# Performance work log

Measured on AMD Instinct MI355X. Metric: run time of the kernel, lower is better.

The kernel has to match this reference:

```python
import jax, jax.numpy as jnp
import numpy as np

B, T, C, HS = 8, 4096, 1024, 128
BLOCK = 4096  # block_size; T == BLOCK here


def _pyr_mask(bs):
    # Faithful numpy translation of the torch 'pyr' buffer construction.
    h = bs // 2
    top = np.repeat(np.flip(np.tril(np.ones((h, h), np.float32)), axis=1), 2, axis=0)  # (bs, h)
    reps = np.array([2] * (h - 1) + [1])
    bot = np.concatenate(
        [np.zeros((1, h), np.float32),
         np.repeat(np.tril(np.ones((h, h), np.float32)), reps, axis=0)], axis=0)  # (bs, h)
    return np.concatenate([top, bot], axis=1)  # (bs, bs)


def setup_inputs() -> dict:
    key = jax.random.key(0)
    kx, kq, kk, kv = jax.random.split(key, 4)
    s = C ** -0.5
    x = jax.random.normal(kx, (B, T, C), jnp.float32)
    Wq = jax.random.normal(kq, (C, HS), jnp.float32) * s
    Wk = jax.random.normal(kk, (C, HS), jnp.float32) * s
    Wv = jax.random.normal(kv, (C, HS), jnp.float32) * s
    return {"x": x, "Wq": Wq, "Wk": Wk, "Wv": Wv}


def reference(x, Wq, Wk, Wv):
    Tlen = x.shape[1]
    start = (BLOCK - Tlen) // 2
    end = BLOCK + (-(BLOCK - Tlen)) // 2  # python floor-div, matches torch slicing
    mask = jnp.asarray(_pyr_mask(BLOCK)[:Tlen, start:end])  # (T, T) 0/1

    q = x @ Wq  # (B, T, HS)
    k = x @ Wk
    v = x @ Wv
    wei = jnp.einsum('btd,bsd->bts', q, k) * (HS ** -0.5)  # (B, T, T)
    wei = jnp.where(mask == 0, -jnp.inf, wei)  # bidirectional_mode == 'bi'
    wei = jax.nn.softmax(wei, axis=-1)
    # dropout p=0.0 -> identity
    return wei @ v  # (B, T, HS)
```

## Files before the change

### kernel.cpp

```cpp
#include <hip/hip_runtime.h>

typedef unsigned short u16;
typedef __attribute__((ext_vector_type(8))) short bf16x8;
typedef __attribute__((ext_vector_type(8))) unsigned short u16x8;
typedef __attribute__((ext_vector_type(4))) float f32x4;
typedef __attribute__((ext_vector_type(4))) unsigned short u16x4;
typedef __attribute__((ext_vector_type(2))) unsigned int u32x2;

#define Bn 8
#define Tn 4096
#define Cn 1024
#define HSn 128

__device__ __forceinline__ float bf2f(u16 b) {
    unsigned u = ((unsigned)b) << 16;
    return __builtin_bit_cast(float, u);
}
__device__ __forceinline__ unsigned cvt_pk_bf16(float a, float b) {
    unsigned r;
    asm("v_cvt_pk_bf16_f32 %0, %1, %2" : "=v"(r) : "v"(a), "v"(b));
    return r;
}
__device__ __forceinline__ u16 f2bf(float f) { return (u16)cvt_pk_bf16(f, f); }

__device__ __forceinline__ void wg_barrier() {
    __builtin_amdgcn_sched_barrier(0);
    asm volatile("s_waitcnt lgkmcnt(0)" ::: "memory");
    __builtin_amdgcn_s_barrier();
    __builtin_amdgcn_sched_barrier(0);
}

extern "C" __global__ __launch_bounds__(256) void head_wtrans(
    const float* __restrict__ Wq, const float* __restrict__ Wk,
    const float* __restrict__ Wv, u16* __restrict__ wt) {
    const float* W = (blockIdx.y == 0) ? Wq : (blockIdx.y == 1) ? Wk : Wv;
    const float scale =
        (blockIdx.y == 0) ? (0.08838834764831845f * 1.4426950408889634f) : 1.0f;
    u16* o = wt + (size_t)blockIdx.y * Cn * HSn;
    int tid = blockIdx.x * 256 + threadIdx.x;
    int n = tid >> 10, kk = tid & 1023;
    o[tid] = f2bf(W[kk * HSn + n] * scale);
}

extern "C" __global__ __launch_bounds__(256) void head_proj(
    const float* __restrict__ x, const u16* __restrict__ wt, u16* __restrict__ qo,
    u16* __restrict__ ko, u16* __restrict__ vto) {
    __shared__ __align__(16) u16 sh[17920];
    u16* const aL = sh;
    u16* const bL = sh + 64 * 40;
    const int tid = threadIdx.x;
    const int w = tid >> 6, l = tid & 63, quad = l >> 4, ln = l & 15;
    const int bm0 = blockIdx.x * 64;

    const f32x4 zero4 = {0.f, 0.f, 0.f, 0.f};
    f32x4 acc[3][2][4];
#pragma unroll
    for (int s = 0; s < 3; s++)
#pragma unroll
        for (int i = 0; i < 2; i++)
#pragma unroll
            for (int j = 0; j < 4; j++) acc[s][i][j] = zero4;

    const int m0w = (w & 1) * 32, n0w = (w >> 1) * 64;

    f32x4 xp[2];
    u16x8 wp[3][2];
    const int xrow[2] = {tid >> 3, (256 + tid) >> 3};
    const int xch = tid & 7;
    const int wrow[2] = {tid >> 2, (256 + tid) >> 2};
    const int wch = tid & 3;

#pragma unroll
    for (int p = 0; p < 2; p++)
        xp[p] = *(const f32x4*)(x + ((size_t)(bm0 + xrow[p])) * Cn + xch * 4);
#pragma unroll
    for (int s = 0; s < 3; s++)
#pragma unroll
        for (int p = 0; p < 2; p++)
            wp[s][p] = *(const u16x8*)(wt + (size_t)s * Cn * HSn + (size_t)wrow[p] * Cn +
                                       wch * 8);

    for (int kt = 0; kt < Cn / 32; kt++) {
        wg_barrier();
#pragma unroll
        for (int p = 0; p < 2; p++) {
            u32x2 d;
            d.x = cvt_pk_bf16(xp[p][0], xp[p][1]);
            d.y = cvt_pk_bf16(xp[p][2], xp[p][3]);
            *(u32x2*)(aL + xrow[p] * 40 + xch * 4) = d;
        }
#pragma unroll
        for (int s = 0; s < 3; s++)
#pragma unroll
            for (int p = 0; p < 2; p++)
                *(u16x8*)(bL + s * 5120 + wrow[p] * 40 + wch * 8) = wp[s][p];
        if (kt + 1 < Cn / 32) {
            const int kn = (kt + 1) * 32;
#pragma unroll
            for (int p = 0; p < 2; p++)
                xp[p] = *(const f32x4*)(x + ((size_t)(bm0 + xrow[p])) * Cn + kn + xch * 4);
#pragma unroll
            for (int s = 0; s < 3; s++)
#pragma unroll
                for (int p = 0; p < 2; p++)
                    wp[s][p] = *(const u16x8*)(wt + (size_t)s * Cn * HSn +
                                               (size_t)wrow[p] * Cn + kn + wch * 8);
        }
        wg_barrier();
        bf16x8 af[2];
#pragma unroll
        for (int mi = 0; mi < 2; mi++)
            af[mi] = *(const bf16x8*)(aL + (m0w + mi * 16 + ln) * 40 + quad * 8);
#pragma unroll
        for (int s = 0; s < 3; s++) {
            bf16x8 bf[4];
#pragma unroll
            for (int ni = 0; ni < 4; ni++)
                bf[ni] =
                    *(const bf16x8*)(bL + s * 5120 + (n0w + ni * 16 + ln) * 40 + quad * 8);
#pragma unroll
            for (int mi = 0; mi < 2; mi++)
#pragma unroll
                for (int ni = 0; ni < 4; ni++)
                    acc[s][mi][ni] = __builtin_amdgcn_mfma_f32_16x16x32_bf16(
                        af[mi], bf[ni], acc[s][mi][ni], 0, 0, 0);
        }
    }
#pragma unroll
    for (int mi = 0; mi < 2; mi++)
#pragma unroll
        for (int ni = 0; ni < 4; ni++)
#pragma unroll
            for (int r = 0; r < 4; r++) {
                int grow = bm0 + m0w + mi * 16 + quad * 4 + r;
                int col = n0w + ni * 16 + ln;
                qo[(size_t)grow * HSn + col] = f2bf(acc[0][mi][ni][r]);
                ko[(size_t)grow * HSn + col] = f2bf(acc[1][mi][ni][r]);
            }
    wg_barrier();
    u16* const tL = sh;
#pragma unroll
    for (int mi = 0; mi < 2; mi++)
#pragma unroll
        for (int ni = 0; ni < 4; ni++) {
            int col = n0w + ni * 16 + ln;
            int trow0 = m0w + mi * 16 + quad * 4;
            u16x4 pk4;
#pragma unroll
            for (int r = 0; r < 4; r++) pk4[r] = f2bf(acc[2][mi][ni][r]);
            *(u16x4*)(tL + col * 80 + trow0) = pk4;
        }
    wg_barrier();
    {
        const int bb = bm0 >> 12, t0b = bm0 & 4095;
        const int dl = tid >> 3, tch = (tid & 7) * 8;
#pragma unroll
        for (int db = 0; db < 4; db++) {
            int d = db * 32 + dl;
            u16x8 vv = *(const u16x8*)(tL + d * 80 + tch);
            *(u16x8*)(vto + ((size_t)bb * HSn + d) * Tn + t0b + tch) = vv;
        }
    }
}

extern "C" __global__ __launch_bounds__(512) void head_flash_chunk(
    const u16* __restrict__ q, const u16* __restrict__ k, const u16* __restrict__ vt,
    u16* __restrict__ Opart, float* __restrict__ lsum) {
    __shared__ __align__(16) u16 kL[64 * 136];
    __shared__ __align__(16) u16 vL[128 * 72];
    __shared__ __align__(16) u16 pL[8 * 16 * 72];
    const int tid = threadIdx.x;
    const int w = tid >> 6, l = tid & 63, quad = l >> 4, ln = l & 15;
    const int cid = blockIdx.x;
    const int grp = cid >> 4;
    const int qbi = (grp < 16) ? (31 - grp) : (grp - 16);
    const int b = (cid >> 1) & 7;
    const int half = cid & 1;
    const int q0 = qbi * 128;
    const int qrow = q0 + w * 16;

    const int rkBase = tid >> 4, ckK = tid & 15;
    const int rvBase = tid >> 3, ckV = tid & 7;

    bf16x8 qf[4];
#pragma unroll
    for (int ks = 0; ks < 4; ks++)
        qf[ks] = *(const bf16x8*)(q + ((size_t)b * Tn + qrow + ln) * HSn + ks * 32 +
                                  quad * 8);

    const f32x4 zero4 = {0.f, 0.f, 0.f, 0.f};
    float l2 = 0.f;
    const int qme = qrow + ln;
    const int clo = 2047 - (qme >> 1), chi = 2047 + ((qme + 1) >> 1);
    const int cloW0 = 2047 - (qrow >> 1);
    const int chiW0 = 2047 + ((qrow + 1) >> 1);
    const int cloMin = 2047 - ((qrow + 15) >> 1);
    const int chiMax = 2047 + ((qrow + 16) >> 1);
    f32x4 o[8];
#pragma unroll
    for (int dt = 0; dt < 8; dt++) o[dt] = zero4;

    const int qmax = q0 + 127;
    const int tlo = (2047 - (qmax >> 1)) >> 6;
    const int thi = (2047 + ((qmax + 1) >> 1)) >> 6;
    const int W = thi - tlo + 1;
    const int c0 = (W + 1) >> 1;
    const int kstart = half ? tlo + c0 : tlo;
    const int kend = half ? thi : tlo + c0 - 1;

    u16x8 pk[2], pv[2];
    {
        const int t0 = kstart * 64;
#pragma unroll
        for (int p = 0; p < 2; p++)
            pk[p] = *(const u16x8*)(k + ((size_t)b * Tn + t0 + p * 32 + rkBase) * HSn +
                                    ckK * 8);
#pragma unroll
        for (int p = 0; p < 2; p++)
            pv[p] = *(const u16x8*)(vt + ((size_t)b * HSn + p * 64 + rvBase) * Tn + t0 +
                                    ckV * 8);
    }

    for (int kt = kstart; kt <= kend; kt++) {
        const int t0 = kt * 64;
        wg_barrier();
#pragma unroll
        for (int p = 0; p < 2; p++)
            *(u16x8*)(kL + (p * 32 + rkBase) * 136 + ckK * 8) = pk[p];
#pragma unroll
        for (int p = 0; p < 2; p++)
            *(u16x8*)(vL + (p * 64 + rvBase) * 72 + ckV * 8) = pv[p];
        if (kt < kend) {
            const int t1 = t0 + 64;
#pragma unroll
            for (int p = 0; p < 2; p++)
                pk[p] = *(const u16x8*)(k + ((size_t)b * Tn + t1 + p * 32 + rkBase) * HSn +
                                        ckK * 8);
#pragma unroll
            for (int p = 0; p < 2; p++)
                pv[p] = *(const u16x8*)(vt + ((size_t)b * HSn + p * 64 + rvBase) * Tn +
                                        t1 + ckV * 8);
        }
        wg_barrier();

        const bool live = !((t0 + 63 < cloMin) || (t0 > chiMax));

        if (live) {
            f32x4 s[4];
#pragma unroll
            for (int nt = 0; nt < 4; nt++) s[nt] = zero4;
            __builtin_amdgcn_s_setprio(1);
#pragma unroll
            for (int nt = 0; nt < 4; nt++) {
                int R = nt * 16 + ln;
#pragma unroll
                for (int ks = 0; ks < 4; ks++) {
                    bf16x8 kf = *(const bf16x8*)(kL + R * 136 + (ks * 4 + quad) * 8);
                    s[nt] =
                        __builtin_amdgcn_mfma_f32_16x16x32_bf16(kf, qf[ks], s[nt], 0, 0, 0);
                }
            }
            __builtin_amdgcn_s_setprio(0);
            if (t0 < cloW0 || t0 + 63 > chiW0) {
#pragma unroll
                for (int nt = 0; nt < 4; nt++)
#pragma unroll
                    for (int r = 0; r < 4; r++) {
                        int t = t0 + nt * 16 + quad * 4 + r;
                        bool valid = (t >= clo) && (t <= chi);
                        s[nt][r] = valid ? s[nt][r] : -1e30f;
                    }
            }
            float ls = 0.f;
#pragma unroll
            for (int nt = 0; nt < 4; nt++) {
                float p0 = exp2f(s[nt][0]), p1 = exp2f(s[nt][1]);
                float p2 = exp2f(s[nt][2]), p3 = exp2f(s[nt][3]);
                ls += (p0 + p1) + (p2 + p3);
                u32x2 d;
                d.x = cvt_pk_bf16(p0, p1);
                d.y = cvt_pk_bf16(p2, p3);
                *(u32x2*)(pL + w * 1152 + ln * 72 + nt * 16 + quad * 4) = d;
            }
            l2 += ls;
            __builtin_amdgcn_s_setprio(1);
#pragma unroll
            for (int jt = 0; jt < 2; jt++) {
                bf16x8 pf = *(const bf16x8*)(pL + w * 1152 + ln * 72 + jt * 32 + quad * 8);
#pragma unroll
                for (int dt = 0; dt < 8; dt++) {
                    int R = dt * 16 + ln;
                    bf16x8 vf = *(const bf16x8*)(vL + R * 72 + (jt * 4 + quad) * 8);
                    o[dt] = __builtin_amdgcn_mfma_f32_16x16x32_bf16(pf, vf, o[dt], 0, 0, 0);
                }
            }
            __builtin_amdgcn_s_setprio(0);
        }
    }
    l2 += __shfl_xor(l2, 16, 64);
    l2 += __shfl_xor(l2, 32, 64);
#pragma unroll
    for (int dt = 0; dt < 8; dt++)
#pragma unroll
        for (int r = 0; r < 4; r++)
            Opart[((size_t)cid * 128 + w * 16 + quad * 4 + r) * HSn + dt * 16 + ln] =
                f2bf(o[dt][r]);
    if (l < 16) lsum[(size_t)cid * 128 + w * 16 + ln] = l2;
}

extern "C" __global__ __launch_bounds__(256) void head_combine(
    const u16* __restrict__ Opart, const float* __restrict__ lsum,
    float* __restrict__ out) {
    const int bid = blockIdx.x;
    const int qb64 = bid >> 3, b = bid & 7;
    const int tid = threadIdx.x;
    const int row = tid >> 2, dseg = (tid & 3) * 32;
    const int qbi = qb64 >> 1;
    const int inrow = (qb64 & 1) * 64 + row;
    const int grp0 = (qbi >= 16) ? (31 - qbi) : (qbi + 16);
    const int cid0 = grp0 * 16 + b * 2;
    const size_t r0 = (size_t)cid0 * 128 + inrow, r1 = r0 + 128;
    float l0 = lsum[r0], l1 = lsum[r1];
    float inv = 1.0f / (l0 + l1);
    float* op = out + ((size_t)b * Tn + qb64 * 64 + row) * HSn + dseg;
    const u16* p0 = Opart + r0 * HSn + dseg;
    const u16* p1 = Opart + r1 * HSn + dseg;
#pragma unroll
    for (int j = 0; j < 4; j++) {
        u16x8 a = *(const u16x8*)(p0 + j * 8);
        u16x8 c = *(const u16x8*)(p1 + j * 8);
        f32x4 o1, o2;
#pragma unroll
        for (int e = 0; e < 4; e++) o1[e] = (bf2f(a[e]) + bf2f(c[e])) * inv;
#pragma unroll
        for (int e = 0; e < 4; e++) o2[e] = (bf2f(a[4 + e]) + bf2f(c[4 + e])) * inv;
        *(f32x4*)(op + j * 8) = o1;
        *(f32x4*)(op + j * 8 + 4) = o2;
    }
}

extern "C" __global__ __launch_bounds__(256) void head_flash(
    const u16* __restrict__ q, const u16* __restrict__ k, const u16* __restrict__ vt,
    float* __restrict__ out) {
    __shared__ __align__(16) u16 kL[64 * 136];
    __shared__ __align__(16) u16 vL[128 * 72];
    __shared__ __align__(16) u16 pL[4 * 16 * 72];
    const int tid = threadIdx.x;
    const int w = tid >> 6, l = tid & 63, quad = l >> 4, ln = l & 15;
    const int bx = blockIdx.x;
    const int half = bx >> 8, idx = bx & 255;
    const int p5 = idx & 31, b = idx >> 5;
    const int qb = half ? p5 : 63 - p5;
    const int q0 = qb * 64;
    const int qrow = q0 + w * 16;
    const int rkBase = tid >> 4, ckK = tid & 15;
    const int rvBase = tid >> 3, ckV = tid & 7;

    bf16x8 qf[4];
#pragma unroll
    for (int ks = 0; ks < 4; ks++)
        qf[ks] = *(const bf16x8*)(q + ((size_t)b * Tn + qrow + ln) * HSn + ks * 32 +
                                  quad * 8);
    const f32x4 zero4 = {0.f, 0.f, 0.f, 0.f};
    float m2 = -1e30f, l2 = 0.f;
    const int qme = qrow + ln;
    const int clo = 2047 - (qme >> 1), chi = 2047 + ((qme + 1) >> 1);
    f32x4 o[8];
#pragma unroll
    for (int dt = 0; dt < 8; dt++) o[dt] = zero4;
    const int qmax = q0 + 63;
    const int tlo = (2047 - (qmax >> 1)) >> 6;
    const int thi = (2047 + ((qmax + 1) >> 1)) >> 6;

    u16x8 pk[4], pv[4];
    {
        const int t0 = tlo * 64;
#pragma unroll
        for (int p = 0; p < 4; p++)
            pk[p] = *(const u16x8*)(k + ((size_t)b * Tn + t0 + p * 16 + rkBase) * HSn +
                                    ckK * 8);
#pragma unroll
        for (int p = 0; p < 4; p++)
            pv[p] = *(const u16x8*)(vt + ((size_t)b * HSn + p * 32 + rvBase) * Tn + t0 +
                                    ckV * 8);
    }
    for (int kt = tlo; kt <= thi; kt++) {
        const int t0 = kt * 64;
        __syncthreads();
#pragma unroll
        for (int p = 0; p < 4; p++)
            *(u16x8*)(kL + (p * 16 + rkBase) * 136 + ckK * 8) = pk[p];
#pragma unroll
        for (int p = 0; p < 4; p++)
            *(u16x8*)(vL + (p * 32 + rvBase) * 72 + ckV * 8) = pv[p];
        if (kt < thi) {
            const int t1 = t0 + 64;
#pragma unroll
            for (int p = 0; p < 4; p++)
                pk[p] = *(const u16x8*)(k + ((size_t)b * Tn + t1 + p * 16 + rkBase) * HSn +
                                        ckK * 8);
#pragma unroll
            for (int p = 0; p < 4; p++)
                pv[p] = *(const u16x8*)(vt + ((size_t)b * HSn + p * 32 + rvBase) * Tn +
                                        t1 + ckV * 8);
        }
        __syncthreads();
        f32x4 s[4];
#pragma unroll
        for (int nt = 0; nt < 4; nt++) s[nt] = zero4;
#pragma unroll
        for (int nt = 0; nt < 4; nt++) {
            int R = nt * 16 + ln;
#pragma unroll
            for (int ks = 0; ks < 4; ks++) {
                bf16x8 kf = *(const bf16x8*)(kL + R * 136 + (ks * 4 + quad) * 8);
                s[nt] = __builtin_amdgcn_mfma_f32_16x16x32_bf16(kf, qf[ks], s[nt], 0, 0, 0);
            }
        }
#pragma unroll
        for (int nt = 0; nt < 4; nt++)
#pragma unroll
            for (int r = 0; r < 4; r++) {
                int t = t0 + nt * 16 + quad * 4 + r;
                bool valid = (t >= clo) && (t <= chi);
                s[nt][r] = valid ? s[nt][r] : -1e30f;
            }
        float mc = s[0][0];
#pragma unroll
        for (int nt = 0; nt < 4; nt++)
#pragma unroll
            for (int r = 0; r < 4; r++) mc = fmaxf(mc, s[nt][r]);
        mc = fmaxf(mc, __shfl_xor(mc, 16, 64));
        mc = fmaxf(mc, __shfl_xor(mc, 32, 64));
        float mn = fmaxf(m2, mc);
        float alpha = exp2f(m2 - mn);
        m2 = mn;
        float ls = 0.f;
#pragma unroll
        for (int nt = 0; nt < 4; nt++) {
            float p0 = exp2f(s[nt][0] - mn), p1 = exp2f(s[nt][1] - mn);
            float p2 = exp2f(s[nt][2] - mn), p3 = exp2f(s[nt][3] - mn);
            ls += (p0 + p1) + (p2 + p3);
            u32x2 d;
            d.x = cvt_pk_bf16(p0, p1);
            d.y = cvt_pk_bf16(p2, p3);
            *(u32x2*)(pL + w * 1152 + ln * 72 + nt * 16 + quad * 4) = d;
        }
        ls += __shfl_xor(ls, 16, 64);
        ls += __shfl_xor(ls, 32, 64);
        l2 = l2 * alpha + ls;
        float aR[4];
#pragma unroll
        for (int r = 0; r < 4; r++) aR[r] = __shfl(alpha, quad * 4 + r, 64);
#pragma unroll
        for (int dt = 0; dt < 8; dt++) {
            f32x4 oo = o[dt];
#pragma unroll
            for (int r = 0; r < 4; r++) oo[r] *= aR[r];
            o[dt] = oo;
        }
#pragma unroll
        for (int jt = 0; jt < 2; jt++) {
            bf16x8 pf = *(const bf16x8*)(pL + w * 1152 + ln * 72 + jt * 32 + quad * 8);
#pragma unroll
            for (int dt = 0; dt < 8; dt++) {
                int R = dt * 16 + ln;
                bf16x8 vf = *(const bf16x8*)(vL + R * 72 + (jt * 4 + quad) * 8);
                o[dt] = __builtin_amdgcn_mfma_f32_16x16x32_bf16(pf, vf, o[dt], 0, 0, 0);
            }
        }
    }
    float inv = 1.0f / l2;
    float rl[4];
#pragma unroll
    for (int r = 0; r < 4; r++) rl[r] = __shfl(inv, quad * 4 + r, 64);
#pragma unroll
    for (int dt = 0; dt < 8; dt++)
#pragma unroll
        for (int r = 0; r < 4; r++) {
            int row = qrow + quad * 4 + r;
            out[((size_t)b * Tn + row) * HSn + dt * 16 + ln] = o[dt][r] * rl[r];
        }
}

extern "C" void kernel_launch(void* const* d_in, const int* in_sizes, int n_in,
                              void* d_out, int out_size, void* d_ws, size_t ws_size,
                              hipStream_t stream) {
    const float* x = (const float*)d_in[0];
    const float* Wq = (const float*)d_in[1];
    const float* Wk = (const float*)d_in[2];
    const float* Wv = (const float*)d_in[3];
    float* outp = (float*)d_out;
    char* ws = (char*)d_ws;
    u16* wt = (u16*)(ws);
    u16* qb = (u16*)(ws + (1u << 20));
    u16* kb = (u16*)(ws + (9u << 20));
    u16* vtb = (u16*)(ws + (17u << 20));
    u16* Opart = (u16*)(ws + (25u << 20));
    float* lsum = (float*)(ws + (42u << 20));

    head_wtrans<<<dim3(512, 3), 256, 0, stream>>>(Wq, Wk, Wv, wt);
    head_proj<<<dim3(512), 256, 0, stream>>>(x, wt, qb, kb, vtb);
    if (ws_size >= (44ull << 20)) {
        head_flash_chunk<<<dim3(512), 512, 0, stream>>>(qb, kb, vtb, Opart, lsum);
        head_combine<<<dim3(512), 256, 0, stream>>>(Opart, lsum, outp);
    } else {
        head_flash<<<dim3(512), 256, 0, stream>>>(qb, kb, vtb, outp);
    }
}
```

Baseline: 295.6 us.

## Load projection operands directly from global into MFMA registers, skipping LDS staging

The QKV projection kernel no longer stages x and weight tiles through shared memory with barriers. Each wave loads its MFMA fragments straight from global memory into registers, converting x to bf16 in registers, and double-buffers the x loads across k-steps. This removes LDS writes, reads and two barriers per k-step. In exchange, weight and x data are no longer shared across waves, so global and L2 traffic rises, and register pressure grows (launch bounds set to one block).

```diff
diff --git a/kernel.cpp b/kernel.cpp
--- a/kernel.cpp
+++ b/kernel.cpp
@@ -6,6 +6,7 @@
 typedef __attribute__((ext_vector_type(4))) float f32x4;
 typedef __attribute__((ext_vector_type(4))) unsigned short u16x4;
 typedef __attribute__((ext_vector_type(2))) unsigned int u32x2;
+typedef __attribute__((ext_vector_type(4))) unsigned int u32x4;
 
 #define Bn 8
 #define Tn 4096
@@ -42,15 +43,14 @@
     o[tid] = f2bf(W[kk * HSn + n] * scale);
 }
 
-extern "C" __global__ __launch_bounds__(256) void head_proj(
+extern "C" __global__ __launch_bounds__(256, 1) void head_proj(
     const float* __restrict__ x, const u16* __restrict__ wt, u16* __restrict__ qo,
     u16* __restrict__ ko, u16* __restrict__ vto) {
-    __shared__ __align__(16) u16 sh[17920];
-    u16* const aL = sh;
-    u16* const bL = sh + 64 * 40;
+    __shared__ __align__(16) u16 tL[128 * 80];
     const int tid = threadIdx.x;
     const int w = tid >> 6, l = tid & 63, quad = l >> 4, ln = l & 15;
     const int bm0 = blockIdx.x * 64;
+    const int m0w = (w & 1) * 32, n0w = (w >> 1) * 64;
 
     const f32x4 zero4 = {0.f, 0.f, 0.f, 0.f};
     f32x4 acc[3][2][4];
@@ -61,71 +61,60 @@
 #pragma unroll
             for (int j = 0; j < 4; j++) acc[s][i][j] = zero4;
 
-    const int m0w = (w & 1) * 32, n0w = (w >> 1) * 64;
-
-    f32x4 xp[2];
-    u16x8 wp[3][2];
-    const int xrow[2] = {tid >> 3, (256 + tid) >> 3};
-    const int xch = tid & 7;
-    const int wrow[2] = {tid >> 2, (256 + tid) >> 2};
-    const int wch = tid & 3;
-
-#pragma unroll
-    for (int p = 0; p < 2; p++)
-        xp[p] = *(const f32x4*)(x + ((size_t)(bm0 + xrow[p])) * Cn + xch * 4);
-#pragma unroll
-    for (int s = 0; s < 3; s++)
-#pragma unroll
-        for (int p = 0; p < 2; p++)
-            wp[s][p] = *(const u16x8*)(wt + (size_t)s * Cn * HSn + (size_t)wrow[p] * Cn +
-                                       wch * 8);
-
-    for (int kt = 0; kt < Cn / 32; kt++) {
-        wg_barrier();
-#pragma unroll
-        for (int p = 0; p < 2; p++) {
-            u32x2 d;
-            d.x = cvt_pk_bf16(xp[p][0], xp[p][1]);
-            d.y = cvt_pk_bf16(xp[p][2], xp[p][3]);
-            *(u32x2*)(aL + xrow[p] * 40 + xch * 4) = d;
-        }
-#pragma unroll
-        for (int s = 0; s < 3; s++)
-#pragma unroll
-            for (int p = 0; p < 2; p++)
-                *(u16x8*)(bL + s * 5120 + wrow[p] * 40 + wch * 8) = wp[s][p];
-        if (kt + 1 < Cn / 32) {
-            const int kn = (kt + 1) * 32;
-#pragma unroll
-            for (int p = 0; p < 2; p++)
-                xp[p] = *(const f32x4*)(x + ((size_t)(bm0 + xrow[p])) * Cn + kn + xch * 4);
-#pragma unroll
-            for (int s = 0; s < 3; s++)
-#pragma unroll
-                for (int p = 0; p < 2; p++)
-                    wp[s][p] = *(const u16x8*)(wt + (size_t)s * Cn * HSn +
-                                               (size_t)wrow[p] * Cn + kn + wch * 8);
-        }
-        wg_barrier();
-        bf16x8 af[2];
-#pragma unroll
-        for (int mi = 0; mi < 2; mi++)
-            af[mi] = *(const bf16x8*)(aL + (m0w + mi * 16 + ln) * 40 + quad * 8);
-#pragma unroll
-        for (int s = 0; s < 3; s++) {
-            bf16x8 bf[4];
-#pragma unroll
-            for (int ni = 0; ni < 4; ni++)
-                bf[ni] =
-                    *(const bf16x8*)(bL + s * 5120 + (n0w + ni * 16 + ln) * 40 + quad * 8);
-#pragma unroll
-            for (int mi = 0; mi < 2; mi++)
-#pragma unroll
-                for (int ni = 0; ni < 4; ni++)
-                    acc[s][mi][ni] = __builtin_amdgcn_mfma_f32_16x16x32_bf16(
-                        af[mi], bf[ni], acc[s][mi][ni], 0, 0, 0);
-        }
-    }
+    const float* xp0 = x + ((size_t)(bm0 + m0w + ln)) * Cn + quad * 8;
+    const float* xp1 = xp0 + (size_t)16 * Cn;
+    const u16* wbase = wt + ((size_t)(n0w + ln)) * Cn + quad * 8;
+
+#define PROJ_LOADX(XC, KT)                             \
+    do {                                               \
+        XC[0][0] = *(const f32x4*)(xp0 + (KT) * 32);   \
+        XC[0][1] = *(const f32x4*)(xp0 + (KT) * 32 + 4); \
+        XC[1][0] = *(const f32x4*)(xp1 + (KT) * 32);   \
+        XC[1][1] = *(const f32x4*)(xp1 + (KT) * 32 + 4); \
+    } while (0)
+
+#define PROJ_LOADW(WB, KT)                                                  \
+    do {                                                                    \
+        _Pragma("unroll") for (int s = 0; s < 3; s++)                       \
+            _Pragma("unroll") for (int ni = 0; ni < 4; ni++)                \
+                WB[s * 4 + ni] = *(const u16x8*)(wbase + (size_t)s * (Cn * HSn) + \
+                                                 ni * (16 * Cn) + (KT) * 32);     \
+    } while (0)
+
+#define PROJ_COMPUTE(XC, WB)                                                   \
+    do {                                                                       \
+        bf16x8 af[2];                                                          \
+        _Pragma("unroll") for (int mi = 0; mi < 2; mi++) {                     \
+            u32x4 t;                                                          \
+            t[0] = cvt_pk_bf16(XC[mi][0][0], XC[mi][0][1]);                    \
+            t[1] = cvt_pk_bf16(XC[mi][0][2], XC[mi][0][3]);                    \
+            t[2] = cvt_pk_bf16(XC[mi][1][0], XC[mi][1][1]);                    \
+            t[3] = cvt_pk_bf16(XC[mi][1][2], XC[mi][1][3]);                    \
+            af[mi] = __builtin_bit_cast(bf16x8, t);                            \
+        }                                                                      \
+        _Pragma("unroll") for (int s = 0; s < 3; s++)                          \
+            _Pragma("unroll") for (int mi = 0; mi < 2; mi++)                   \
+                _Pragma("unroll") for (int ni = 0; ni < 4; ni++)               \
+                    acc[s][mi][ni] = __builtin_amdgcn_mfma_f32_16x16x32_bf16(  \
+                        af[mi], __builtin_bit_cast(bf16x8, WB[s * 4 + ni]),    \
+                        acc[s][mi][ni], 0, 0, 0);                              \
+    } while (0)
+
+    f32x4 xA[2][2], xB[2][2];
+    u16x8 wb[12];
+    PROJ_LOADX(xA, 0);
+    for (int kt = 0; kt < 32; kt += 2) {
+        PROJ_LOADW(wb, kt);
+        PROJ_LOADX(xB, kt + 1);
+        PROJ_COMPUTE(xA, wb);
+        PROJ_LOADW(wb, kt + 1);
+        if (kt + 2 < 32) PROJ_LOADX(xA, kt + 2);
+        PROJ_COMPUTE(xB, wb);
+    }
+#undef PROJ_LOADX
+#undef PROJ_LOADW
+#undef PROJ_COMPUTE
+
 #pragma unroll
     for (int mi = 0; mi < 2; mi++)
 #pragma unroll
@@ -137,8 +126,6 @@
                 qo[(size_t)grow * HSn + col] = f2bf(acc[0][mi][ni][r]);
                 ko[(size_t)grow * HSn + col] = f2bf(acc[1][mi][ni][r]);
             }
-    wg_barrier();
-    u16* const tL = sh;
 #pragma unroll
     for (int mi = 0; mi < 2; mi++)
 #pragma unroll
```

Result: slower. 365.4 us (+23.6%).
